# Optimization experiments

Hardware: AMD Instinct MI355X
Metric: run time of the kernel (lower is better)

Reference implementation:

```python
import jax, jax.numpy as jnp
import numpy as np

IN_FEATURE = 256
OUT_FEATURE = 128
ALPHA = 0.5  # LeakyReLU negative slope
NEG_BIG = -9e15


def setup_inputs() -> dict:
    key = jax.random.key(0)
    k1, k2, k3, k4 = jax.random.split(key, 4)
    N = 8192
    x = jax.random.normal(k1, (N, IN_FEATURE), dtype=jnp.float32)
    adj = jax.random.randint(k2, (N, N), 0, 2, dtype=jnp.int32)
    stdv = 1.0 / np.sqrt(OUT_FEATURE)
    W = jax.random.uniform(k3, (IN_FEATURE, OUT_FEATURE), dtype=jnp.float32,
                           minval=-stdv, maxval=stdv)
    a = jax.random.uniform(k4, (2 * OUT_FEATURE, 1), dtype=jnp.float32,
                           minval=-stdv, maxval=stdv)
    return {"input": x, "adj": adj, "W": W, "a": a}


def reference(input, adj, W, a):
    # h: [N, F_out]
    h = input @ W
    # Additive attention: cat([h_i, h_j]) @ a == h_i @ a1 + h_j @ a2
    a1 = a[:OUT_FEATURE, 0]   # [F_out]
    a2 = a[OUT_FEATURE:, 0]   # [F_out]
    f1 = h @ a1               # [N]  (row / source contribution)
    f2 = h @ a2               # [N]  (col / target contribution)
    e = jax.nn.leaky_relu(f1[:, None] + f2[None, :], negative_slope=ALPHA)  # [N, N]
    scores = jnp.where(adj > 0, e, NEG_BIG)
    attention = jax.nn.softmax(scores, axis=1)  # [N, N]
    h_prime = attention @ h                     # [N, F_out]
    return jax.nn.elu(h_prime)
```

## Files before the change

### kernel.cpp

```cpp
#include <hip/hip_runtime.h>

#define N_NODES 8192
#define IN_F 256
#define OUT_F 128
#define ALPHA 0.5f
#define JC 4
#define KCHUNK 2048
#define RK 128
#define ROUNDS 16
#define RSTEPS 4

using short8 = __attribute__((ext_vector_type(8))) short;
using f32x4  = __attribute__((ext_vector_type(4))) float;

__device__ __forceinline__ unsigned int f2bf(float f){
  unsigned int u = __float_as_uint(f);
  u += 0x7fffu + ((u >> 16) & 1u);
  return u >> 16;
}
__device__ __forceinline__ float bf2f(short s){
  return __uint_as_float(((unsigned int)(unsigned short)s) << 16);
}

__global__ __launch_bounds__(256) void k_hfp(const float* __restrict__ x,
                                             const float* __restrict__ W,
                                             const float* __restrict__ a,
                                             unsigned short* __restrict__ P,
                                             float* __restrict__ f1,
                                             float* __restrict__ f2){
  __shared__ float xs[16*IN_F];
  const int tid = threadIdx.x;
  const int bx = blockIdx.x;
  const int r0 = bx * 16;
  const float4* xg = (const float4*)(x + (size_t)r0*IN_F);
  float4* xl = (float4*)xs;
  #pragma unroll
  for(int i=0;i<4;i++) xl[tid + i*256] = xg[tid + i*256];
  __syncthreads();
  const int wave = tid >> 6, lane = tid & 63;
  float2 acc[4];
  #pragma unroll
  for(int j=0;j<4;j++){ acc[j].x = 0.f; acc[j].y = 0.f; }
  const float2* Wp = (const float2*)W;
  for(int k4=0;k4<IN_F;k4+=4){
    float4 xq[4];
    #pragma unroll
    for(int j=0;j<4;j++) xq[j] = *(const float4*)&xs[(wave*4+j)*IN_F + k4];
    #pragma unroll
    for(int kk=0;kk<4;kk++){
      float2 wv = Wp[(size_t)(k4+kk)*64 + lane];
      #pragma unroll
      for(int j=0;j<4;j++){
        float xv = kk==0?xq[j].x : kk==1?xq[j].y : kk==2?xq[j].z : xq[j].w;
        acc[j].x += xv*wv.x; acc[j].y += xv*wv.y;
      }
    }
  }
  float2 av1 = ((const float2*)a)[lane];
  float2 av2 = ((const float2*)(a + OUT_F))[lane];
  #pragma unroll
  for(int j=0;j<4;j++){
    float s1 = acc[j].x*av1.x + acc[j].y*av1.y;
    float s2 = acc[j].x*av2.x + acc[j].y*av2.y;
    #pragma unroll
    for(int off=32; off; off>>=1){
      s1 += __shfl_down(s1, off);
      s2 += __shfl_down(s2, off);
    }
    if(lane == 0){ f1[r0 + wave*4 + j] = s1; f2[r0 + wave*4 + j] = s2; }
  }
  __syncthreads();
  #pragma unroll
  for(int j=0;j<4;j++) *(float2*)&xs[(wave*4+j)*132 + lane*2] = acc[j];
  __syncthreads();
  const int kb = bx >> 1, half = bx & 1;
  const int c = tid >> 5, ql = (tid >> 4) & 1, n = tid & 15;
  short8 v;
  #pragma unroll
  for(int t=0;t<8;t++) v[t] = (short)f2bf(xs[(ql*8+t)*132 + c*16 + n]);
  *(short8*)(P + ((size_t)((kb*8 + c)*64 + half*32 + ql*16 + n))*8) = v;
}

__global__ __launch_bounds__(256, 2) void k_attn(const int* __restrict__ adj,
    const unsigned short* __restrict__ P,
    const float* __restrict__ f1, const float* __restrict__ f2,
    float* __restrict__ part, float* __restrict__ denp){
  __shared__ __align__(16) unsigned short Alds[64*RK];
  __shared__ __align__(16) short Blds[RK*OUT_F];
  __shared__ float f1s[64];
  const int tid = threadIdx.x;
  const int wave = tid >> 6, lane = tid & 63;
  const int m = lane & 15, q = lane >> 4;
  const int jc = blockIdx.x;
  const int r0b = blockIdx.y * 64;
  const int jb = jc * KCHUNK;
  const int kb0 = jc * (KCHUNK/32);
  const int srow = tid >> 5;
  const int sc0  = (tid & 31) * 4;
  const int swz  = ((((sc0 >> 3) ^ srow) << 4) | ((sc0 & 4) << 1));

  if(tid < 64) f1s[tid] = f1[r0b + tid];

  f32x4 acc0[8];
  #pragma unroll
  for(int c=0;c<8;c++) acc0[c] = (f32x4){0,0,0,0};
  float den0 = 0.f;

  const char* Ab = (const char*)Alds;
  char* Aw = (char*)Alds + swz;
  const int mw = m & 7;
  const int rg0 = wave*16 + m;

  __syncthreads();

  for(int rd=0; rd<ROUNDS; rd++){
    const int kbase = jb + rd*RK;
    const int4* Pb = (const int4*)(P + ((size_t)(kb0 + rd*4) << 12));
    int4* Bl4 = (int4*)Blds;
    #pragma unroll
    for(int i=0;i<8;i++) Bl4[i*256 + tid] = Pb[i*256 + tid];
    float4 fv = *(const float4*)(f2 + kbase + sc0);
    const char* ap = (const char*)adj + (((size_t)(r0b + srow)*N_NODES + kbase + sc0) << 2);
    #pragma unroll
    for(int i=0;i<8;i++){
      int4 av = *(const int4*)(ap + ((size_t)i*8*N_NODES << 2));
      float f1v = f1s[i*8 + srow];
      float t0 = f1v + fv.x, t1 = f1v + fv.y, t2 = f1v + fv.z, t3 = f1v + fv.w;
      t0 = t0 > 0.f ? t0 : ALPHA*t0;  t1 = t1 > 0.f ? t1 : ALPHA*t1;
      t2 = t2 > 0.f ? t2 : ALPHA*t2;  t3 = t3 > 0.f ? t3 : ALPHA*t3;
      float w0 = av.x > 0 ? __expf(t0) : 0.f;
      float w1 = av.y > 0 ? __expf(t1) : 0.f;
      float w2 = av.z > 0 ? __expf(t2) : 0.f;
      float w3 = av.w > 0 ? __expf(t3) : 0.f;
      uint2 pk;
      pk.x = f2bf(w0) | (f2bf(w1) << 16);
      pk.y = f2bf(w2) | (f2bf(w3) << 16);
      *(uint2*)(Aw + (i*8 + srow)*(RK*2)) = pk;
    }
    __syncthreads();
    #pragma unroll
    for(int s=0;s<RSTEPS;s++){
      const int gq = ((s*4 + q) ^ mw) << 4;
      short8 A0 = *(const short8*)(Ab + rg0*(RK*2) + gq);
      #pragma unroll
      for(int t=0;t<8;t++) den0 += bf2f(A0[t]);
      const short8* Bl = (const short8*)Blds + s*512 + lane;
      #pragma unroll
      for(int c=0;c<8;c++){
        short8 Bf = Bl[c*64];
        acc0[c] = __builtin_amdgcn_mfma_f32_16x16x32_bf16(A0, Bf, acc0[c], 0,0,0);
      }
    }
    __syncthreads();
  }

  den0 += __shfl_down(den0, 32); den0 += __shfl_down(den0, 16);
  const int r0w = r0b + wave*16;
  if(lane < 16) denp[(size_t)jc*N_NODES + r0w + lane] = den0;
  float* pp = part + (size_t)jc*N_NODES*OUT_F;
  #pragma unroll
  for(int c=0;c<8;c++){
    #pragma unroll
    for(int reg=0;reg<4;reg++)
      pp[(size_t)(r0w + q*4 + reg)*OUT_F + c*16 + m] = acc0[c][reg];
  }
}

__global__ __launch_bounds__(256) void k_out(const float* __restrict__ part,
    const float* __restrict__ denp, float* __restrict__ out){
  const int idx = blockIdx.x*256 + threadIdx.x;
  const int r = idx >> 7;
  float v = 0.f, d = 0.f;
  #pragma unroll
  for(int p=0;p<JC;p++){
    v += part[(size_t)p*N_NODES*OUT_F + idx];
    d += denp[(size_t)p*N_NODES + r];
  }
  v /= d;
  out[idx] = v > 0.f ? v : (__expf(v) - 1.f);
}

extern "C" void kernel_launch(void* const* d_in, const int* in_sizes, int n_in,
                              void* d_out, int out_size, void* d_ws, size_t ws_size,
                              hipStream_t stream){
  const float* x   = (const float*)d_in[0];
  const int*   adj = (const int*)d_in[1];
  const float* W   = (const float*)d_in[2];
  const float* a   = (const float*)d_in[3];
  char* ws = (char*)d_ws;
  unsigned short* P = (unsigned short*)ws;
  float* f1         = (float*)(ws + (2u<<20));
  float* f2         = (float*)(ws + (2u<<20) + (32u<<10));
  float* part       = (float*)(ws + (4u<<20));
  float* denp       = (float*)(ws + (20u<<20));
  float* out        = (float*)d_out;

  k_hfp<<<512, 256, 0, stream>>>(x, W, a, P, f1, f2);
  k_attn<<<dim3(JC,128), 256, 0, stream>>>(adj, P, f1, f2, part, denp);
  k_out<<<(N_NODES*OUT_F)/256, 256, 0, stream>>>(part, denp, out);
}
```

Baseline: 398.9 us.

## Drop LDS staging in attention kernel; compute A fragments in registers with prefetch

```diff
diff --git a/kernel.cpp b/kernel.cpp
--- a/kernel.cpp
+++ b/kernel.cpp
@@ -6,9 +6,7 @@
 #define ALPHA 0.5f
 #define JC 4
 #define KCHUNK 2048
-#define RK 128
-#define ROUNDS 16
-#define RSTEPS 4
+#define STEPS (KCHUNK/32)
 
 using short8 = __attribute__((ext_vector_type(8))) short;
 using f32x4  = __attribute__((ext_vector_type(4))) float;
@@ -85,99 +83,91 @@
     const unsigned short* __restrict__ P,
     const float* __restrict__ f1, const float* __restrict__ f2,
     float* __restrict__ part, float* __restrict__ denp){
-  __shared__ __align__(16) unsigned short Alds[64*RK];
-  __shared__ __align__(16) short Blds[RK*OUT_F];
-  __shared__ float f1s[64];
   const int tid = threadIdx.x;
   const int wave = tid >> 6, lane = tid & 63;
   const int m = lane & 15, q = lane >> 4;
   const int jc = blockIdx.x;
-  const int r0b = blockIdx.y * 64;
+  const int r0w = blockIdx.y * 64 + wave*16;
   const int jb = jc * KCHUNK;
-  const int kb0 = jc * (KCHUNK/32);
-  const int srow = tid >> 5;
-  const int sc0  = (tid & 31) * 4;
-  const int swz  = ((((sc0 >> 3) ^ srow) << 4) | ((sc0 & 4) << 1));
+  const int kb0 = jc * STEPS;
 
-  if(tid < 64) f1s[tid] = f1[r0b + tid];
+  const float f1v = f1[r0w + m];
+  f32x4 acc[8];
+  #pragma unroll
+  for(int c=0;c<8;c++) acc[c] = (f32x4){0,0,0,0};
+  float den = 0.f;
 
-  f32x4 acc0[8];
-  #pragma unroll
-  for(int c=0;c<8;c++) acc0[c] = (f32x4){0,0,0,0};
-  float den0 = 0.f;
+  const char* aprow = (const char*)adj + ((size_t)(r0w + m)*N_NODES + jb + q*8)*4;
+  const float* f2p = f2 + jb + q*8;
+  const short8* P8 = (const short8*)P;
 
-  const char* Ab = (const char*)Alds;
-  char* Aw = (char*)Alds + swz;
-  const int mw = m & 7;
-  const int rg0 = wave*16 + m;
+  int4 a0 = *(const int4*)(aprow);
+  int4 a1 = *(const int4*)(aprow + 16);
+  float4 g0 = *(const float4*)(f2p);
+  float4 g1 = *(const float4*)(f2p + 4);
 
-  __syncthreads();
-
-  for(int rd=0; rd<ROUNDS; rd++){
-    const int kbase = jb + rd*RK;
-    const int4* Pb = (const int4*)(P + ((size_t)(kb0 + rd*4) << 12));
-    int4* Bl4 = (int4*)Blds;
+  for(int s=0; s<STEPS; s++){
+    const short8* Bs = P8 + ((size_t)(kb0 + s)*8)*64 + lane;
+    short8 bf[8];
     #pragma unroll
-    for(int i=0;i<8;i++) Bl4[i*256 + tid] = Pb[i*256 + tid];
-    float4 fv = *(const float4*)(f2 + kbase + sc0);
-    const char* ap = (const char*)adj + (((size_t)(r0b + srow)*N_NODES + kbase + sc0) << 2);
+    for(int c=0;c<8;c++) bf[c] = Bs[c*64];
+    const int sn = (s+1 < STEPS) ? s+1 : s;
+    int4 na0 = *(const int4*)(aprow + (size_t)sn*128);
+    int4 na1 = *(const int4*)(aprow + (size_t)sn*128 + 16);
+    float4 ng0 = *(const float4*)(f2p + sn*32);
+    float4 ng1 = *(const float4*)(f2p + sn*32 + 4);
+    float e0 = f1v + g0.x; e0 = e0>0.f?e0:ALPHA*e0; float w0 = a0.x>0?__expf(e0):0.f;
+    float e1 = f1v + g0.y; e1 = e1>0.f?e1:ALPHA*e1; float w1 = a0.y>0?__expf(e1):0.f;
+    float e2 = f1v + g0.z; e2 = e2>0.f?e2:ALPHA*e2; float w2 = a0.z>0?__expf(e2):0.f;
+    float e3 = f1v + g0.w; e3 = e3>0.f?e3:ALPHA*e3; float w3 = a0.w>0?__expf(e3):0.f;
+    float e4 = f1v + g1.x; e4 = e4>0.f?e4:ALPHA*e4; float w4 = a1.x>0?__expf(e4):0.f;
+    float e5 = f1v + g1.y; e5 = e5>0.f?e5:ALPHA*e5; float w5 = a1.y>0?__expf(e5):0.f;
+    float e6 = f1v + g1.z; e6 = e6>0.f?e6:ALPHA*e6; float w6 = a1.z>0?__expf(e6):0.f;
+    float e7 = f1v + g1.w; e7 = e7>0.f?e7:ALPHA*e7; float w7 = a1.w>0?__expf(e7):0.f;
+    uint4 pk;
+    pk.x = f2bf(w0) | (f2bf(w1) << 16);
+    pk.y = f2bf(w2) | (f2bf(w3) << 16);
+    pk.z = f2bf(w4) | (f2bf(w5) << 16);
+    pk.w = f2bf(w6) | (f2bf(w7) << 16);
+    short8 af = __builtin_bit_cast(short8, pk);
     #pragma unroll
-    for(int i=0;i<8;i++){
-      int4 av = *(const int4*)(ap + ((size_t)i*8*N_NODES << 2));
-      float f1v = f1s[i*8 + srow];
-      float t0 = f1v + fv.x, t1 = f1v + fv.y, t2 = f1v + fv.z, t3 = f1v + fv.w;
-      t0 = t0 > 0.f ? t0 : ALPHA*t0;  t1 = t1 > 0.f ? t1 : ALPHA*t1;
-      t2 = t2 > 0.f ? t2 : ALPHA*t2;  t3 = t3 > 0.f ? t3 : ALPHA*t3;
-      float w0 = av.x > 0 ? __expf(t0) : 0.f;
-      float w1 = av.y > 0 ? __expf(t1) : 0.f;
-      float w2 = av.z > 0 ? __expf(t2) : 0.f;
-      float w3 = av.w > 0 ? __expf(t3) : 0.f;
-      uint2 pk;
-      pk.x = f2bf(w0) | (f2bf(w1) << 16);
-      pk.y = f2bf(w2) | (f2bf(w3) << 16);
-      *(uint2*)(Aw + (i*8 + srow)*(RK*2)) = pk;
-    }
-    __syncthreads();
+    for(int t=0;t<8;t++) den += bf2f(af[t]);
     #pragma unroll
-    for(int s=0;s<RSTEPS;s++){
-      const int gq = ((s*4 + q) ^ mw) << 4;
-      short8 A0 = *(const short8*)(Ab + rg0*(RK*2) + gq);
-      #pragma unroll
-      for(int t=0;t<8;t++) den0 += bf2f(A0[t]);
-      const short8* Bl = (const short8*)Blds + s*512 + lane;
-      #pragma unroll
-      for(int c=0;c<8;c++){
-        short8 Bf = Bl[c*64];
-        acc0[c] = __builtin_amdgcn_mfma_f32_16x16x32_bf16(A0, Bf, acc0[c], 0,0,0);
-      }
-    }
-    __syncthreads();
+    for(int c=0;c<8;c++)
+      acc[c] = __builtin_amdgcn_mfma_f32_16x16x32_bf16(af, bf[c], acc[c], 0,0,0);
+    a0 = na0; a1 = na1; g0 = ng0; g1 = ng1;
   }
 
-  den0 += __shfl_down(den0, 32); den0 += __shfl_down(den0, 16);
-  const int r0w = r0b + wave*16;
-  if(lane < 16) denp[(size_t)jc*N_NODES + r0w + lane] = den0;
+  den += __shfl_down(den, 32); den += __shfl_down(den, 16);
+  if(lane < 16) denp[(size_t)jc*N_NODES + r0w + lane] = den;
   float* pp = part + (size_t)jc*N_NODES*OUT_F;
   #pragma unroll
   for(int c=0;c<8;c++){
     #pragma unroll
     for(int reg=0;reg<4;reg++)
-      pp[(size_t)(r0w + q*4 + reg)*OUT_F + c*16 + m] = acc0[c][reg];
+      pp[(size_t)(r0w + q*4 + reg)*OUT_F + c*16 + m] = acc[c][reg];
   }
 }
 
 __global__ __launch_bounds__(256) void k_out(const float* __restrict__ part,
     const float* __restrict__ denp, float* __restrict__ out){
   const int idx = blockIdx.x*256 + threadIdx.x;
-  const int r = idx >> 7;
-  float v = 0.f, d = 0.f;
+  const int r = idx >> 5;
+  float4 v = {0.f,0.f,0.f,0.f};
+  float d = 0.f;
   #pragma unroll
   for(int p=0;p<JC;p++){
-    v += part[(size_t)p*N_NODES*OUT_F + idx];
+    float4 pv = *((const float4*)part + (size_t)p*(N_NODES*OUT_F/4) + idx);
+    v.x += pv.x; v.y += pv.y; v.z += pv.z; v.w += pv.w;
     d += denp[(size_t)p*N_NODES + r];
   }
-  v /= d;
-  out[idx] = v > 0.f ? v : (__expf(v) - 1.f);
+  float4 o;
+  o.x = v.x/d; o.y = v.y/d; o.z = v.z/d; o.w = v.w/d;
+  o.x = o.x>0.f ? o.x : (__expf(o.x)-1.f);
+  o.y = o.y>0.f ? o.y : (__expf(o.y)-1.f);
+  o.z = o.z>0.f ? o.z : (__expf(o.z)-1.f);
+  o.w = o.w>0.f ? o.w : (__expf(o.w)-1.f);
+  *((float4*)out + idx) = o;
 }
 
 extern "C" void kernel_launch(void* const* d_in, const int* in_sizes, int n_in,
@@ -197,5 +187,5 @@
 
   k_hfp<<<512, 256, 0, stream>>>(x, W, a, P, f1, f2);
   k_attn<<<dim3(JC,128), 256, 0, stream>>>(adj, P, f1, f2, part, denp);
-  k_out<<<(N_NODES*OUT_F)/256, 256, 0, stream>>>(part, denp, out);
+  k_out<<<(N_NODES*OUT_F)/4/256, 256, 0, stream>>>(part, denp, out);
 }
```

After: 576.1 us. +44.4%, slower.
